# Kernel optimization log

Hardware: AMD Instinct MI355X
Metric: run time of the kernel (lower is better)

Reference implementation:

```python
import jax, jax.numpy as jnp
import numpy as np

N = 20000      # num_atoms
C = 64         # num_features (channels)
I = 16         # num_irreps = (l_max+1)^2, l_max=3
K2, K1, K0 = 120, 8, 4  # CG basis sizes per correlation order


def setup_inputs() -> dict:
    key = jax.random.key(0)
    ks = jax.random.split(key, 7)
    return {
        "node_feats": jax.random.normal(ks[0], (N, C, I), jnp.float32),
        "U2": jax.random.normal(ks[1], (I, I, I, K2), jnp.float32),
        "U1": jax.random.normal(ks[2], (I, I, K1), jnp.float32),
        "U0": jax.random.normal(ks[3], (I, K0), jnp.float32),
        "w2": jax.random.normal(ks[4], (K2, C), jnp.float32),
        "w1": jax.random.normal(ks[5], (K1, C), jnp.float32),
        "w0": jax.random.normal(ks[6], (K0, C), jnp.float32),
    }


def reference(node_feats, U2, U1, U0, w2, w1, w0):
    # equation_main: '...ik,kc,bci -> bc...' with U2 [I,I,I,K2]
    # -> out [N, C, I, I]
    out = jnp.einsum('xyik,kc,nci->ncxy', U2, w2, node_feats)

    # corr = 1: weighting '...k,kc->c...' then contract 'bc...i,bci->bc...'
    c1 = jnp.einsum('xik,kc->cxi', U1, w1)          # [C, I, I]
    out = jnp.einsum('ncxi,nci->ncx', c1 + out, node_feats)  # [N, C, I]

    # corr = 0
    c0 = jnp.einsum('ik,kc->ci', U0, w0)            # [C, I]
    out = jnp.einsum('nci,nci->nc', c0 + out, node_feats)    # [N, C]
    return out
```

## Files before the change

### kernel.cpp

```cpp
#include <hip/hip_runtime.h>

#define NATOMS 20000
#define NCHAN  64
#define NIRR   16
#define K2 120
#define K1 8
#define K0 4

#define W1_BYTE_OFF 524288
#define W0_BYTE_OFF 557056

typedef __attribute__((ext_vector_type(8))) short bf16x8;
typedef __attribute__((ext_vector_type(4))) float f32x4;
typedef __attribute__((ext_vector_type(4))) unsigned int u32x4;

__device__ inline short f2bf(float f) {
    union { float f; unsigned u; } v; v.f = f;
    unsigned r = v.u + 0x7FFF + ((v.u >> 16) & 1);
    return (short)(r >> 16);
}

__global__ __launch_bounds__(256) void precompute_kernel(
    const float* __restrict__ U2, const float* __restrict__ U1,
    const float* __restrict__ U0, const float* __restrict__ w2,
    const float* __restrict__ w1, const float* __restrict__ w0,
    void* __restrict__ wsv)
{
    short* W2bf = (short*)wsv;
    short* W1bf = (short*)((char*)wsv + W1_BYTE_OFF);
    float* W0f  = (float*)((char*)wsv + W0_BYTE_OFF);

    const int b = blockIdx.x;
    const int t = threadIdx.x;

    if (b < 256) {
        __shared__ __align__(16) float U2s[64][121];
        __shared__ __align__(16) float w2s[120][16];
        const int xyi0  = (b >> 2) * 64;
        const int cbase = (b & 3) * 16;

        for (int o = t; o < 64 * 120; o += 256) {
            int r = o / 120, k = o - r * 120;
            U2s[r][k] = U2[(size_t)xyi0 * 120 + o];
        }
        for (int o = t; o < 120 * 16; o += 256) {
            int k = o >> 4, cc = o & 15;
            w2s[k][cc] = w2[k * NCHAN + cbase + cc];
        }
        __syncthreads();

        const int r = t & 63;
        const int g = t >> 6;
        float acc0 = 0.f, acc1 = 0.f, acc2 = 0.f, acc3 = 0.f;
        #pragma unroll 8
        for (int k = 0; k < 120; ++k) {
            float u = U2s[r][k];
            float4 w = *(const float4*)&w2s[k][g * 4];
            acc0 += u * w.x; acc1 += u * w.y; acc2 += u * w.z; acc3 += u * w.w;
        }
        const int xyi = xyi0 + r;
        const int cA  = cbase + g * 4;
        W2bf[(size_t)(cA + 0) * 4096 + xyi] = f2bf(acc0);
        W2bf[(size_t)(cA + 1) * 4096 + xyi] = f2bf(acc1);
        W2bf[(size_t)(cA + 2) * 4096 + xyi] = f2bf(acc2);
        W2bf[(size_t)(cA + 3) * 4096 + xyi] = f2bf(acc3);
    } else {
        const int lb = b - 256;
        for (int o = t; o < 2048; o += 256) {
            int go = lb * 2048 + o;
            int c = go >> 8, xy = go & 255;
            const float* u = U1 + xy * K1;
            float acc = 0.f;
            #pragma unroll
            for (int k = 0; k < K1; ++k) acc += u[k] * w1[k * NCHAN + c];
            W1bf[c * 256 + xy] = f2bf(acc);
        }
        if (lb == 0) {
            for (int o = t; o < 1024; o += 256) {
                int c = o >> 4, x = o & 15;
                const float* u = U0 + x * K0;
                float acc = 0.f;
                #pragma unroll
                for (int k = 0; k < K0; ++k) acc += u[k] * w0[k * NCHAN + c];
                W0f[c * 16 + x] = acc;
            }
        }
    }
}

__device__ __forceinline__ void compute_tile(
    const bf16x8 (&aw)[16], float4 c0, int q,
    float4 va, float4 vb, float4 vc, float4 vd,
    float* __restrict__ outp)
{
    float f0 = va.x, f1 = va.y, f2 = va.z, f3 = va.w;
    float f4 = vb.x, f5 = vb.y, f6 = vb.z, f7 = vb.w;
    float f8 = vc.x, f9 = vc.y, f10 = vc.z, f11 = vc.w;
    float f12 = vd.x, f13 = vd.y, f14 = vd.z, f15 = vd.w;

    unsigned pk0, pk1, pk2, pk3, pk4, pk5, pk6, pk7;
    asm("v_cvt_pk_bf16_f32 %0, %1, %2" : "=v"(pk0) : "v"(f0),  "v"(f1));
    asm("v_cvt_pk_bf16_f32 %0, %1, %2" : "=v"(pk1) : "v"(f2),  "v"(f3));
    asm("v_cvt_pk_bf16_f32 %0, %1, %2" : "=v"(pk2) : "v"(f4),  "v"(f5));
    asm("v_cvt_pk_bf16_f32 %0, %1, %2" : "=v"(pk3) : "v"(f6),  "v"(f7));
    asm("v_cvt_pk_bf16_f32 %0, %1, %2" : "=v"(pk4) : "v"(f8),  "v"(f9));
    asm("v_cvt_pk_bf16_f32 %0, %1, %2" : "=v"(pk5) : "v"(f10), "v"(f11));
    asm("v_cvt_pk_bf16_f32 %0, %1, %2" : "=v"(pk6) : "v"(f12), "v"(f13));
    asm("v_cvt_pk_bf16_f32 %0, %1, %2" : "=v"(pk7) : "v"(f14), "v"(f15));

    unsigned w0s = (q == 0) ? pk0 : (q == 1) ? pk4 : (q == 2) ? 0x00003f80u : 0u;
    unsigned w1s = (q == 0) ? pk1 : (q == 1) ? pk5 : 0u;
    unsigned w2s_ = (q == 0) ? pk2 : (q == 1) ? pk6 : 0u;
    unsigned w3s = (q == 0) ? pk3 : (q == 1) ? pk7 : 0u;
    u32x4 bu = {w0s, w1s, w2s_, w3s};
    bf16x8 bfr = __builtin_bit_cast(bf16x8, bu);

    const f32x4 z = {0.f, 0.f, 0.f, 0.f};
    f32x4 sy = z;
    f32x4 d0 = __builtin_amdgcn_mfma_f32_16x16x32_bf16(aw[0], bfr, z, 0, 0, 0);
    f32x4 d1 = __builtin_amdgcn_mfma_f32_16x16x32_bf16(aw[1], bfr, z, 0, 0, 0);
    f32x4 d2 = __builtin_amdgcn_mfma_f32_16x16x32_bf16(aw[2], bfr, z, 0, 0, 0);
    f32x4 d3 = __builtin_amdgcn_mfma_f32_16x16x32_bf16(aw[3], bfr, z, 0, 0, 0);
    sy += d0 * f0;  d0 = __builtin_amdgcn_mfma_f32_16x16x32_bf16(aw[4],  bfr, z, 0, 0, 0);
    sy += d1 * f1;  d1 = __builtin_amdgcn_mfma_f32_16x16x32_bf16(aw[5],  bfr, z, 0, 0, 0);
    sy += d2 * f2;  d2 = __builtin_amdgcn_mfma_f32_16x16x32_bf16(aw[6],  bfr, z, 0, 0, 0);
    sy += d3 * f3;  d3 = __builtin_amdgcn_mfma_f32_16x16x32_bf16(aw[7],  bfr, z, 0, 0, 0);
    sy += d0 * f4;  d0 = __builtin_amdgcn_mfma_f32_16x16x32_bf16(aw[8],  bfr, z, 0, 0, 0);
    sy += d1 * f5;  d1 = __builtin_amdgcn_mfma_f32_16x16x32_bf16(aw[9],  bfr, z, 0, 0, 0);
    sy += d2 * f6;  d2 = __builtin_amdgcn_mfma_f32_16x16x32_bf16(aw[10], bfr, z, 0, 0, 0);
    sy += d3 * f7;  d3 = __builtin_amdgcn_mfma_f32_16x16x32_bf16(aw[11], bfr, z, 0, 0, 0);
    sy += d0 * f8;  d0 = __builtin_amdgcn_mfma_f32_16x16x32_bf16(aw[12], bfr, z, 0, 0, 0);
    sy += d1 * f9;  d1 = __builtin_amdgcn_mfma_f32_16x16x32_bf16(aw[13], bfr, z, 0, 0, 0);
    sy += d2 * f10; d2 = __builtin_amdgcn_mfma_f32_16x16x32_bf16(aw[14], bfr, z, 0, 0, 0);
    sy += d3 * f11; d3 = __builtin_amdgcn_mfma_f32_16x16x32_bf16(aw[15], bfr, z, 0, 0, 0);
    sy += d0 * f12; sy += d1 * f13; sy += d2 * f14; sy += d3 * f15;

    float t0 = (q & 1) ? f4 : f0;   float u0 = (q & 1) ? f12 : f8;
    float fy0 = (q & 2) ? u0 : t0;
    float t1 = (q & 1) ? f5 : f1;   float u1 = (q & 1) ? f13 : f9;
    float fy1 = (q & 2) ? u1 : t1;
    float t2 = (q & 1) ? f6 : f2;   float u2 = (q & 1) ? f14 : f10;
    float fy2 = (q & 2) ? u2 : t2;
    float t3 = (q & 1) ? f7 : f3;   float u3 = (q & 1) ? f15 : f11;
    float fy3 = (q & 2) ? u3 : t3;

    float s = fy0 * (sy.x + c0.x);
    s = fmaf(fy1, sy.y + c0.y, s);
    s = fmaf(fy2, sy.z + c0.z, s);
    s = fmaf(fy3, sy.w + c0.w, s);
    s += __shfl_xor(s, 16);
    s += __shfl_xor(s, 32);
    if (q == 0) *outp = s;
}

__global__ __launch_bounds__(256, 3) void contract_kernel(
    const float* __restrict__ nf,
    const void* __restrict__ wsv,
    float* __restrict__ out)
{
    const short* W2g = (const short*)wsv;
    const short* W1g = (const short*)((const char*)wsv + W1_BYTE_OFF);
    const float* W0g = (const float*)((const char*)wsv + W0_BYTE_OFF);

    const int tid  = threadIdx.x;
    const int wave = tid >> 6;
    const int lane = tid & 63;
    const int m    = lane & 15;
    const int q    = lane >> 4;
    const int c    = blockIdx.x * 4 + wave;
    const int chunk = blockIdx.y;

    bf16x8 aw[16];
    #pragma unroll
    for (int j = 0; j < 16; ++j) {
        bf16x8 v = (bf16x8)0;
        if (q < 2) {
            v = *(const bf16x8*)(W2g + ((size_t)c << 12) + ((j * 16 + m) << 4) + (q << 3));
        } else if (q == 2) {
            v[0] = W1g[(c << 8) + (j << 4) + m];
        }
        aw[j] = v;
    }
    const float4 c0 = *(const float4*)(W0g + (c << 4) + (q << 2));

    const float* fbase = nf + ((size_t)chunk * 160 + m) * 1024 + c * 16;
    float* obase = out + ((size_t)chunk * 160 + m) * 64 + c;

    float4 a0, a1, a2, a3, e0, e1, e2, e3;
    {
        const float4* p = (const float4*)fbase;
        a0 = p[0]; a1 = p[1]; a2 = p[2]; a3 = p[3];
    }
    for (int T = 0; T < 10; T += 2) {
        {
            const float4* p = (const float4*)(fbase + (size_t)(T + 1) * 16384);
            e0 = p[0]; e1 = p[1]; e2 = p[2]; e3 = p[3];
        }
        compute_tile(aw, c0, q, a0, a1, a2, a3, obase + (size_t)T * 1024);
        {
            int Tn = (T + 2 < 10) ? (T + 2) : 0;
            const float4* p = (const float4*)(fbase + (size_t)Tn * 16384);
            a0 = p[0]; a1 = p[1]; a2 = p[2]; a3 = p[3];
        }
        compute_tile(aw, c0, q, e0, e1, e2, e3, obase + (size_t)(T + 1) * 1024);
    }
}

extern "C" void kernel_launch(void* const* d_in, const int* in_sizes, int n_in,
                              void* d_out, int out_size, void* d_ws, size_t ws_size,
                              hipStream_t stream)
{
    const float* nf = (const float*)d_in[0];
    const float* U2 = (const float*)d_in[1];
    const float* U1 = (const float*)d_in[2];
    const float* U0 = (const float*)d_in[3];
    const float* w2 = (const float*)d_in[4];
    const float* w1 = (const float*)d_in[5];
    const float* w0 = (const float*)d_in[6];
    float* out = (float*)d_out;

    precompute_kernel<<<264, 256, 0, stream>>>(U2, U1, U0, w2, w1, w0, d_ws);

    dim3 grid(16, 125);
    contract_kernel<<<grid, 256, 0, stream>>>(nf, d_ws, out);
}
```

Before: 180.1 us.

## Stage node features through LDS with async global_load_lds double buffering

The contract kernel now uses 512-thread blocks covering 8 channels, and it loads node-feature tiles cooperatively into a swizzled, double-buffered LDS array using global_load_lds. Each wave then reads its 16 irreps from LDS. Outputs are held in registers and written after the loop. The goal is fully coalesced 512-byte row loads in place of strided per-lane float4 loads, with the next tile's load overlapping compute. The cost is two block barriers per tile and extra LDS traffic.

```diff
diff --git a/kernel.cpp b/kernel.cpp
--- a/kernel.cpp
+++ b/kernel.cpp
@@ -9,6 +9,8 @@
 
 #define W1_BYTE_OFF 524288
 #define W0_BYTE_OFF 557056
+
+#define NT 10
 
 typedef __attribute__((ext_vector_type(8))) short bf16x8;
 typedef __attribute__((ext_vector_type(4))) float f32x4;
@@ -88,10 +90,15 @@
     }
 }
 
-__device__ __forceinline__ void compute_tile(
+__device__ __forceinline__ void gload_lds16(const void* g, void* l) {
+    __builtin_amdgcn_global_load_lds(
+        (const __attribute__((address_space(1))) unsigned int*)g,
+        (__attribute__((address_space(3))) unsigned int*)l, 16, 0, 0);
+}
+
+__device__ __forceinline__ float compute_tile(
     const bf16x8 (&aw)[16], float4 c0, int q,
-    float4 va, float4 vb, float4 vc, float4 vd,
-    float* __restrict__ outp)
+    float4 va, float4 vb, float4 vc, float4 vd)
 {
     float f0 = va.x, f1 = va.y, f2 = va.z, f3 = va.w;
     float f4 = vb.x, f5 = vb.y, f6 = vb.z, f7 = vb.w;
@@ -150,14 +157,16 @@
     s = fmaf(fy3, sy.w + c0.w, s);
     s += __shfl_xor(s, 16);
     s += __shfl_xor(s, 32);
-    if (q == 0) *outp = s;
-}
-
-__global__ __launch_bounds__(256, 3) void contract_kernel(
+    return s;
+}
+
+__global__ __launch_bounds__(512, 3) void contract_kernel(
     const float* __restrict__ nf,
     const void* __restrict__ wsv,
     float* __restrict__ out)
 {
+    __shared__ __align__(16) float fs[2][2048];
+
     const short* W2g = (const short*)wsv;
     const short* W1g = (const short*)((const char*)wsv + W1_BYTE_OFF);
     const float* W0g = (const float*)((const char*)wsv + W0_BYTE_OFF);
@@ -167,8 +176,17 @@
     const int lane = tid & 63;
     const int m    = lane & 15;
     const int q    = lane >> 4;
-    const int c    = blockIdx.x * 4 + wave;
+    const int c    = blockIdx.x * 8 + wave;
     const int chunk = blockIdx.y;
+
+    const int a_st = tid >> 5;
+    const int soff = ((tid & 31) << 4) ^ ((a_st & 7) << 4);
+    const char* sbase = (const char*)nf
+        + ((size_t)(chunk * 160 + a_st) << 12)
+        + ((size_t)blockIdx.x << 9)
+        + soff;
+    char* ldst0 = (char*)&fs[0][0] + (wave << 10);
+    char* ldst1 = (char*)&fs[1][0] + (wave << 10);
 
     bf16x8 aw[16];
     #pragma unroll
@@ -183,26 +201,38 @@
     }
     const float4 c0 = *(const float4*)(W0g + (c << 4) + (q << 2));
 
-    const float* fbase = nf + ((size_t)chunk * 160 + m) * 1024 + c * 16;
-    float* obase = out + ((size_t)chunk * 160 + m) * 64 + c;
-
-    float4 a0, a1, a2, a3, e0, e1, e2, e3;
-    {
-        const float4* p = (const float4*)fbase;
-        a0 = p[0]; a1 = p[1]; a2 = p[2]; a3 = p[3];
-    }
-    for (int T = 0; T < 10; T += 2) {
-        {
-            const float4* p = (const float4*)(fbase + (size_t)(T + 1) * 16384);
-            e0 = p[0]; e1 = p[1]; e2 = p[2]; e3 = p[3];
-        }
-        compute_tile(aw, c0, q, a0, a1, a2, a3, obase + (size_t)T * 1024);
-        {
-            int Tn = (T + 2 < 10) ? (T + 2) : 0;
-            const float4* p = (const float4*)(fbase + (size_t)Tn * 16384);
-            a0 = p[0]; a1 = p[1]; a2 = p[2]; a3 = p[3];
-        }
-        compute_tile(aw, c0, q, e0, e1, e2, e3, obase + (size_t)(T + 1) * 1024);
+    const unsigned sw = (unsigned)((m & 7) << 4);
+    const unsigned zb = (unsigned)(wave << 6);
+
+    float outv[NT];
+
+    gload_lds16(sbase, ldst0);
+
+    #pragma unroll
+    for (int T = 0; T < NT; ++T) {
+        const int b = T & 1;
+        if (T + 1 < NT)
+            gload_lds16(sbase + (size_t)(T + 1) * 65536, b ? ldst0 : ldst1);
+        if (T + 1 < NT) { asm volatile("s_waitcnt vmcnt(1)" ::: "memory"); }
+        else            { asm volatile("s_waitcnt vmcnt(0)" ::: "memory"); }
+        __builtin_amdgcn_s_barrier();
+
+        const char* lrb = (const char*)&fs[b][0] + (m << 9);
+        float4 va = *(const float4*)(lrb + ((zb +  0) ^ sw));
+        float4 vb = *(const float4*)(lrb + ((zb + 16) ^ sw));
+        float4 vc = *(const float4*)(lrb + ((zb + 32) ^ sw));
+        float4 vd = *(const float4*)(lrb + ((zb + 48) ^ sw));
+
+        outv[T] = compute_tile(aw, c0, q, va, vb, vc, vd);
+
+        __builtin_amdgcn_s_barrier();
+    }
+
+    if (q == 0) {
+        float* ob = out + ((size_t)(chunk * 160 + m)) * 64 + c;
+        #pragma unroll
+        for (int T = 0; T < NT; ++T)
+            ob[(size_t)T * 1024] = outv[T];
     }
 }
 
@@ -221,6 +251,6 @@
 
     precompute_kernel<<<264, 256, 0, stream>>>(U2, U1, U0, w2, w1, w0, d_ws);
 
-    dim3 grid(16, 125);
-    contract_kernel<<<grid, 256, 0, stream>>>(nf, d_ws, out);
-}
+    dim3 grid(8, 125);
+    contract_kernel<<<grid, 512, 0, stream>>>(nf, d_ws, out);
+}
```

After: 176.2 us. 1.02x faster.
